# Performance work log

Hardware: AMD Instinct MI355X
Metric: run time of the kernel (lower is better)

The kernel has to match this reference:

```python
import jax, jax.numpy as jnp
import numpy as np

B, N, M, C = 32, 4096, 512, 256  # batch, grid points, retained modes, latent channels


def setup_inputs() -> dict:
    key = jax.random.key(0)
    k1, k2 = jax.random.split(key)
    v = jax.random.normal(k1, (B, N, C), dtype=jnp.float32)
    # glorot-style scale for a (C, C) per-mode transform: std = 1/sqrt(C)
    transform_R = jax.random.normal(k2, (M, C, C), dtype=jnp.float32) * np.float32(1.0 / np.sqrt(C))
    return {"v": v, "transform_R": transform_R}


def reference(v, transform_R):
    # v: (B, N, C) real; transform_R: (M, C, C) real, applied to complex modes
    n = v.shape[1]
    m = transform_R.shape[0]
    f = jnp.fft.rfft(v, axis=1)                     # (B, N//2+1, C) complex64
    fm = f[:, :m]                                   # keep low-frequency modes (B, M, C)
    # per-mode channel mixing: out[b,m,o] = sum_i R[m,i,o] * f[b,m,i]
    gm = jnp.einsum('mio,bmi->bmo', transform_R.astype(fm.dtype), fm)
    g = jnp.zeros_like(f).at[:, :m].set(gm)         # zero-pad high modes back
    return v + jnp.fft.irfft(g, n=n, axis=1)        # residual add, (B, N, C)
```

## Files before the change

### kernel.cpp

```cpp
#include <hip/hip_runtime.h>
#include <hip/hip_fp16.h>
#include <math.h>


constexpr int BB = 32;
constexpr int CC = 256;
constexpr int MM = 512;

constexpr float PI2_4096 = 1.5339807878856412e-3f;
constexpr float PI2_512  = 1.2271846303085130e-2f;
constexpr float PI2_64   = 9.8174770424681035e-2f;
constexpr float PI_4     = 0.78539816339744831f;

__device__ __forceinline__ float2 cadd(float2 a, float2 b){ return make_float2(a.x+b.x, a.y+b.y); }
__device__ __forceinline__ float2 csub(float2 a, float2 b){ return make_float2(a.x-b.x, a.y-b.y); }
__device__ __forceinline__ float2 cmulf(float2 a, float2 b){ return make_float2(a.x*b.x - a.y*b.y, a.x*b.y + a.y*b.x); }

template<int S>
__device__ __forceinline__ void dif8(float2 x[8]) {
    const float R = 0.70710678118654752f;
    const float Sf = (float)S;
    float2 a0=cadd(x[0],x[4]), a1=cadd(x[1],x[5]), a2=cadd(x[2],x[6]), a3=cadd(x[3],x[7]);
    float2 d0=csub(x[0],x[4]), d1=csub(x[1],x[5]), d2=csub(x[2],x[6]), d3=csub(x[3],x[7]);
    float2 t5 = cmulf(d1, make_float2(R, -R*Sf));
    float2 t6 = make_float2(Sf*d2.y, -Sf*d2.x);
    float2 t7 = cmulf(d3, make_float2(-R, -R*Sf));
    float2 b0=cadd(a0,a2), b1=cadd(a1,a3), b2=csub(a0,a2), e3=csub(a1,a3);
    float2 b3=make_float2(Sf*e3.y, -Sf*e3.x);
    float2 b4=cadd(d0,t6), b5=cadd(t5,t7), b6=csub(d0,t6), e7=csub(t5,t7);
    float2 b7=make_float2(Sf*e7.y, -Sf*e7.x);
    x[0]=cadd(b0,b1); x[4]=csub(b0,b1);
    x[2]=cadd(b2,b3); x[6]=csub(b2,b3);
    x[1]=cadd(b4,b5); x[5]=csub(b4,b5);
    x[3]=cadd(b6,b7); x[7]=csub(b6,b7);
}

__device__ __forceinline__ void twid7(float2 x[8], float ang) {
    float s, c;
    __sincosf(ang, &s, &c);
    float2 w = make_float2(c, s), cur = w;
    x[1] = cmulf(x[1], cur);
    #pragma unroll
    for (int k = 2; k < 8; ++k) { cur = cmulf(cur, w); x[k] = cmulf(x[k], cur); }
}

__global__ __launch_bounds__(256) void k1a_kernel(const float* __restrict__ v,
                                                  __half2* __restrict__ ybuf, int b0) {
    __shared__ float2 T[64 * 65];
    const int blk = blockIdx.x;
    const int ct = blk & 1;
    const int n2 = (blk >> 1) & 63;
    const int bl = blk >> 7;
    const int bat = b0 + bl;
    const int t = threadIdx.x;
    const int p = t & 63;
    const int g = t >> 6;

    const float* vb = v + ((size_t)bat << 20) + (size_t)n2 * CC + ct * 128 + 2 * p;
    float2 X[2][8];
    #pragma unroll
    for (int s = 0; s < 2; ++s) {
        const int bd = g + 4 * s;
        #pragma unroll
        for (int a = 0; a < 8; ++a)
            X[s][a] = *(const float2*)(vb + (size_t)(8 * a + bd) * 16384);
    }
    #pragma unroll
    for (int s = 0; s < 2; ++s) {
        const int bd = g + 4 * s;
        dif8<1>(X[s]);
        twid7(X[s], -PI2_64 * (float)bd);
        float2* row = T + p * 65;
        #pragma unroll
        for (int k0 = 0; k0 < 8; ++k0) row[bd + 8 * k0] = X[s][k0];
    }
    __syncthreads();

    __half2* yb = ybuf + (size_t)bl * (64 * 64 * 128) + ct * 64 + p;
    #pragma unroll
    for (int s = 0; s < 2; ++s) {
        const int k0 = g + 4 * s;
        float2 Y[8];
        const float2* row = T + p * 65 + 8 * k0;
        #pragma unroll
        for (int b = 0; b < 8; ++b) Y[b] = row[b];
        dif8<1>(Y);
        float bs, bc, ss, sc;
        __sincosf(-PI2_4096 * (float)(n2 * k0), &bs, &bc);
        __sincosf(-PI2_512 * (float)n2, &ss, &sc);
        float2 cur = make_float2(bc, bs), stp = make_float2(sc, ss);
        #pragma unroll
        for (int k1b = 0; k1b < 8; ++k1b) {
            float2 r = cmulf(Y[k1b], cur);
            yb[(size_t)((k0 + 8 * k1b) * 64 + n2) * 128] = __floats2half2_rn(r.x, r.y);
            cur = cmulf(cur, stp);
        }
    }
}

__global__ __launch_bounds__(256) void k1b_kernel(const __half2* __restrict__ ybuf,
                                                  __half2* __restrict__ zbuf, int b0) {
    __shared__ float2 T[64 * 65];
    const int blk = blockIdx.x;
    const int ct = blk & 1;
    const int k1 = (blk >> 1) & 63;
    const int bl = blk >> 7;
    const int bat = b0 + bl;
    const int t = threadIdx.x;
    const int p = t & 63;
    const int g = t >> 6;
    const float R = 0.70710678118654752f;

    const __half2* yb = ybuf + (size_t)bl * (64 * 64 * 128) + (size_t)k1 * (64 * 128) + ct * 64 + p;
    float2 X[2][8];
    #pragma unroll
    for (int s = 0; s < 2; ++s) {
        const int bd = g + 4 * s;
        #pragma unroll
        for (int a = 0; a < 8; ++a)
            X[s][a] = __half22float2(yb[(size_t)(8 * a + bd) * 128]);
    }
    #pragma unroll
    for (int s = 0; s < 2; ++s) {
        const int bd = g + 4 * s;
        dif8<1>(X[s]);
        twid7(X[s], -PI2_64 * (float)bd);
        float2* row = T + p * 65;
        #pragma unroll
        for (int k0 = 0; k0 < 8; ++k0) row[bd + 8 * k0] = X[s][k0];
    }
    __syncthreads();

    __half2* zb = zbuf + ((size_t)(bat * 64 + k1) * 16) * 128 + ct * 64 + p;
    #pragma unroll
    for (int s = 0; s < 2; ++s) {
        const int k20 = g + 4 * s;
        float2 r[8];
        const float2* row = T + p * 65 + 8 * k20;
        #pragma unroll
        for (int b = 0; b < 8; ++b) r[b] = row[b];
        float2 sum0 = make_float2(0.f, 0.f);
        #pragma unroll
        for (int b = 0; b < 8; ++b) sum0 = cadd(sum0, r[b]);
        float2 e0 = csub(r[0], r[4]);
        float2 e1 = csub(r[1], r[5]);
        float2 e2 = csub(r[2], r[6]);
        float2 e3 = csub(r[3], r[7]);
        float2 sum7 = cadd(cadd(e0, cmulf(e1, make_float2(R, R))),
                           cadd(make_float2(-e2.y, e2.x), cmulf(e3, make_float2(-R, R))));
        zb[(size_t)k20 * 128]       = __floats2half2_rn(sum0.x, sum0.y);
        zb[(size_t)(k20 + 8) * 128] = __floats2half2_rn(sum7.x, sum7.y);
    }
}

__global__ __launch_bounds__(256) void k2_kernel(const __half2* __restrict__ zbuf,
                                                 const float* __restrict__ R,
                                                 __half* __restrict__ gre,
                                                 __half* __restrict__ gim) {
    __shared__ __half XT[256 * 64];
    const int mh = blockIdx.x & 1;
    const int m  = blockIdx.x >> 1;
    const int t = threadIdx.x;
    const int k1 = m & 63, k2 = m >> 6;
    int k1p, jp;
    if (k1 == 0) { k1p = 0;       jp = (k2 == 0) ? 0 : (16 - k2); }
    else         { k1p = 64 - k1; jp = 15 - k2; }
    {
        const int b  = t & 31;
        const int pg = t >> 5;
        const __half2* zm = zbuf + ((size_t)(b * 64 + k1 ) * 16 + k2) * 128;
        const __half2* zp = zbuf + ((size_t)(b * 64 + k1p) * 16 + jp) * 128;
        #pragma unroll
        for (int q = 0; q < 16; ++q) {
            int pp = pg + 8 * q;
            float2 a = __half22float2(zm[pp]);
            float2 c = __half22float2(zp[pp]);
            XT[(2 * pp) * 64 + b]          = __float2half_rn(0.5f * (a.x + c.x));
            XT[(2 * pp) * 64 + 32 + b]     = __float2half_rn(0.5f * (a.y - c.y));
            XT[(2 * pp + 1) * 64 + b]      = __float2half_rn(0.5f * (a.y + c.y));
            XT[(2 * pp + 1) * 64 + 32 + b] = __float2half_rn(0.5f * (c.x - a.x));
        }
    }
    __syncthreads();

    const int rblk = t >> 4;
    const int ol   = t & 15;
    float4 acc[2][4];
    #pragma unroll
    for (int jj = 0; jj < 2; ++jj)
        #pragma unroll
        for (int rr = 0; rr < 4; ++rr) acc[jj][rr] = make_float4(0.f, 0.f, 0.f, 0.f);

    const float* Rb = R + (size_t)m * 65536 + mh * 128 + ol * 4;
    float4 c0 = *(const float4*)&Rb[0];
    float4 c1 = *(const float4*)&Rb[64];
    for (int i = 0; i < 256; ++i) {
        float4 n0 = c0, n1 = c1;
        if (i < 255) {
            n0 = *(const float4*)&Rb[(size_t)(i + 1) * 256];
            n1 = *(const float4*)&Rb[(size_t)(i + 1) * 256 + 64];
        }
        const __half2* xp = (const __half2*)&XT[i * 64 + rblk * 4];
        float2 x01 = __half22float2(xp[0]);
        float2 x23 = __half22float2(xp[1]);
        float xs[4] = {x01.x, x01.y, x23.x, x23.y};
        #pragma unroll
        for (int rr = 0; rr < 4; ++rr) {
            acc[0][rr].x += xs[rr] * c0.x; acc[0][rr].y += xs[rr] * c0.y;
            acc[0][rr].z += xs[rr] * c0.z; acc[0][rr].w += xs[rr] * c0.w;
            acc[1][rr].x += xs[rr] * c1.x; acc[1][rr].y += xs[rr] * c1.y;
            acc[1][rr].z += xs[rr] * c1.z; acc[1][rr].w += xs[rr] * c1.w;
        }
        c0 = n0; c1 = n1;
    }

    union U { __half2 h2[2]; float2 f2; };
    #pragma unroll
    for (int jj = 0; jj < 2; ++jj) {
        #pragma unroll
        for (int rr = 0; rr < 4; ++rr) {
            int r = rblk * 4 + rr;
            __half* plane = (r < 32) ? gre : gim;
            size_t off = ((size_t)m * BB + (r & 31)) * CC + mh * 128 + (ol + 16 * jj) * 4;
            U u;
            u.h2[0] = __floats2half2_rn(acc[jj][rr].x, acc[jj][rr].y);
            u.h2[1] = __floats2half2_rn(acc[jj][rr].z, acc[jj][rr].w);
            *(float2*)(plane + off) = u.f2;
        }
    }
}

__global__ __launch_bounds__(256) void k3a_kernel(const __half* __restrict__ gre,
                                                  const __half* __restrict__ gim,
                                                  __half2* __restrict__ tbuf, int b0) {
    const int blk = blockIdx.x;
    const int ct = blk & 1;
    const int k1 = (blk >> 1) & 63;
    const int bl = blk >> 7;
    const int bat = b0 + bl;
    const int t = threadIdx.x;
    const int p = t & 63;
    const int g = t >> 6;

    float2 Zd[8], Zc[8];
    #pragma unroll
    for (int k20 = 0; k20 < 8; ++k20) {
        int m = k1 + 64 * k20;
        size_t off = ((size_t)m * BB + bat) * CC + ct * 128 + 2 * p;
        float2 a = __half22float2(*(const __half2*)(gre + off));
        float2 c = __half22float2(*(const __half2*)(gim + off));
        Zd[k20] = make_float2(a.x - c.y, c.x + a.y);
        int mp = 512 - k1 - 64 * k20;
        if (mp != 512) {
            size_t offp = ((size_t)mp * BB + bat) * CC + ct * 128 + 2 * p;
            float2 ap = __half22float2(*(const __half2*)(gre + offp));
            float2 cp = __half22float2(*(const __half2*)(gim + offp));
            Zc[k20] = make_float2(ap.x + cp.y, ap.y - cp.x);
        } else {
            Zc[k20] = make_float2(0.f, 0.f);
        }
    }

    __half2* tb = tbuf + (size_t)bl * (64 * 64 * 128) + (size_t)k1 * 128 + ct * 64 + p;
    #pragma unroll
    for (int s = 0; s < 2; ++s) {
        const int bd = g + 4 * s;
        float w8s, w8c;
        __sincosf(-PI_4 * (float)bd, &w8s, &w8c);
        float2 u[8];
        #pragma unroll
        for (int k20 = 0; k20 < 8; ++k20)
            u[k20] = cadd(Zd[k20], cmulf(Zc[k20], make_float2(w8c, w8s)));
        twid7(u, PI2_64 * (float)bd);
        dif8<-1>(u);
        float bs, bc, ss, sc;
        __sincosf(PI2_4096 * (float)(bd * k1), &bs, &bc);
        __sincosf(PI2_512 * (float)k1, &ss, &sc);
        float2 cur = make_float2(bc, bs), stp = make_float2(sc, ss);
        #pragma unroll
        for (int a = 0; a < 8; ++a) {
            float2 r = cmulf(u[a], cur);
            tb[(size_t)(8 * a + bd) * (64 * 128)] = __floats2half2_rn(r.x, r.y);
            cur = cmulf(cur, stp);
        }
    }
}

__global__ __launch_bounds__(256) void k3b_kernel(const __half2* __restrict__ tbuf,
                                                  const float* __restrict__ v,
                                                  float* __restrict__ out, int b0) {
    __shared__ float2 T[64 * 65];
    const int blk = blockIdx.x;
    const int ct = blk & 1;
    const int n2 = (blk >> 1) & 63;
    const int bl = blk >> 7;
    const int bat = b0 + bl;
    const int t = threadIdx.x;
    const int p = t & 63;
    const int g = t >> 6;

    const __half2* tb = tbuf + (size_t)bl * (64 * 64 * 128) + (size_t)n2 * (64 * 128) + ct * 64 + p;
    float2 X[2][8];
    #pragma unroll
    for (int s = 0; s < 2; ++s) {
        const int be = g + 4 * s;
        #pragma unroll
        for (int a = 0; a < 8; ++a)
            X[s][a] = __half22float2(tb[(size_t)(8 * a + be) * 128]);
    }
    #pragma unroll
    for (int s = 0; s < 2; ++s) {
        const int be = g + 4 * s;
        dif8<-1>(X[s]);
        twid7(X[s], PI2_64 * (float)be);
        float2* row = T + p * 65;
        #pragma unroll
        for (int j0 = 0; j0 < 8; ++j0) row[be + 8 * j0] = X[s][j0];
    }
    __syncthreads();

    const float sc = 1.0f / 4096.0f;
    const float* vb = v   + ((size_t)bat << 20) + (size_t)n2 * CC + ct * 128 + 2 * p;
    float*       ob = out + ((size_t)bat << 20) + (size_t)n2 * CC + ct * 128 + 2 * p;
    #pragma unroll
    for (int s = 0; s < 2; ++s) {
        const int j0 = g + 4 * s;
        float2 r[8];
        const float2* row = T + p * 65 + 8 * j0;
        #pragma unroll
        for (int b = 0; b < 8; ++b) r[b] = row[b];
        dif8<-1>(r);
        #pragma unroll
        for (int j1 = 0; j1 < 8; ++j1) {
            int n1 = j0 + 8 * j1;
            size_t off = (size_t)n1 * 16384;
            float2 vz = *(const float2*)(vb + off);
            float2 o = make_float2(vz.x + r[j1].x * sc, vz.y + r[j1].y * sc);
            *(float2*)(ob + off) = o;
        }
    }
}

extern "C" void kernel_launch(void* const* d_in, const int* in_sizes, int n_in,
                              void* d_out, int out_size, void* d_ws, size_t ws_size,
                              hipStream_t stream) {
    const float* v = (const float*)d_in[0];
    const float* R = (const float*)d_in[1];
    float* out = (float*)d_out;

    __half2* ybuf = (__half2*)d_ws;
    __half2* zbuf = ybuf + (size_t)16 * 64 * 64 * 128;
    __half*  gre  = (__half*)(zbuf + (size_t)32 * 64 * 16 * 128);
    __half*  gim  = gre + (size_t)MM * BB * CC;

    for (int h = 0; h < 2; ++h) {
        k1a_kernel<<<2048, 256, 0, stream>>>(v, ybuf, h * 16);
        k1b_kernel<<<2048, 256, 0, stream>>>(ybuf, zbuf, h * 16);
    }
    k2_kernel<<<1024, 256, 0, stream>>>(zbuf, R, gre, gim);
    for (int h = 0; h < 2; ++h) {
        k3a_kernel<<<2048, 256, 0, stream>>>(gre, gim, ybuf, h * 16);
        k3b_kernel<<<2048, 256, 0, stream>>>(ybuf, v, out, h * 16);
    }
}
```

Before: 485.7 us.

## Use fp16 MFMA with split hi/lo weights for per-mode channel mixing

Replaces the scalar FMA loop in the per-mode channel-mixing kernel with MFMA 16x16x32 fp16 instructions. The activation tile is stored transposed in shared memory with an XOR swizzle to avoid bank conflicts. The fp32 weights are split into high and low fp16 parts so two MFMAs keep roughly fp32 accuracy. The aim is to move the matmul onto the matrix cores instead of the vector ALUs. In exchange it adds strided, uncoalesced weight loads and scalar half stores on output.

```diff
diff --git a/kernel.cpp b/kernel.cpp
--- a/kernel.cpp
+++ b/kernel.cpp
@@ -11,6 +11,9 @@
 constexpr float PI2_512  = 1.2271846303085130e-2f;
 constexpr float PI2_64   = 9.8174770424681035e-2f;
 constexpr float PI_4     = 0.78539816339744831f;
+
+typedef _Float16 f16x8 __attribute__((ext_vector_type(8)));
+typedef float f32x4 __attribute__((ext_vector_type(4)));
 
 __device__ __forceinline__ float2 cadd(float2 a, float2 b){ return make_float2(a.x+b.x, a.y+b.y); }
 __device__ __forceinline__ float2 csub(float2 a, float2 b){ return make_float2(a.x-b.x, a.y-b.y); }
@@ -153,11 +156,15 @@
     }
 }
 
+__device__ __forceinline__ int swzh(int r, int col) {
+    return r * 256 + (col ^ ((r & 7) << 3));
+}
+
 __global__ __launch_bounds__(256) void k2_kernel(const __half2* __restrict__ zbuf,
                                                  const float* __restrict__ R,
                                                  __half* __restrict__ gre,
                                                  __half* __restrict__ gim) {
-    __shared__ __half XT[256 * 64];
+    __shared__ __align__(16) __half XT[64 * 256];
     const int mh = blockIdx.x & 1;
     const int m  = blockIdx.x >> 1;
     const int t = threadIdx.x;
@@ -175,57 +182,64 @@
             int pp = pg + 8 * q;
             float2 a = __half22float2(zm[pp]);
             float2 c = __half22float2(zp[pp]);
-            XT[(2 * pp) * 64 + b]          = __float2half_rn(0.5f * (a.x + c.x));
-            XT[(2 * pp) * 64 + 32 + b]     = __float2half_rn(0.5f * (a.y - c.y));
-            XT[(2 * pp + 1) * 64 + b]      = __float2half_rn(0.5f * (a.y + c.y));
-            XT[(2 * pp + 1) * 64 + 32 + b] = __float2half_rn(0.5f * (c.x - a.x));
+            *(__half2*)&XT[swzh(b,      2 * pp)] = __floats2half2_rn(0.5f * (a.x + c.x), 0.5f * (a.y + c.y));
+            *(__half2*)&XT[swzh(b + 32, 2 * pp)] = __floats2half2_rn(0.5f * (a.y - c.y), 0.5f * (c.x - a.x));
         }
     }
     __syncthreads();
 
-    const int rblk = t >> 4;
-    const int ol   = t & 15;
-    float4 acc[2][4];
-    #pragma unroll
-    for (int jj = 0; jj < 2; ++jj)
-        #pragma unroll
-        for (int rr = 0; rr < 4; ++rr) acc[jj][rr] = make_float4(0.f, 0.f, 0.f, 0.f);
-
-    const float* Rb = R + (size_t)m * 65536 + mh * 128 + ol * 4;
-    float4 c0 = *(const float4*)&Rb[0];
-    float4 c1 = *(const float4*)&Rb[64];
-    for (int i = 0; i < 256; ++i) {
-        float4 n0 = c0, n1 = c1;
-        if (i < 255) {
-            n0 = *(const float4*)&Rb[(size_t)(i + 1) * 256];
-            n1 = *(const float4*)&Rb[(size_t)(i + 1) * 256 + 64];
-        }
-        const __half2* xp = (const __half2*)&XT[i * 64 + rblk * 4];
-        float2 x01 = __half22float2(xp[0]);
-        float2 x23 = __half22float2(xp[1]);
-        float xs[4] = {x01.x, x01.y, x23.x, x23.y};
-        #pragma unroll
-        for (int rr = 0; rr < 4; ++rr) {
-            acc[0][rr].x += xs[rr] * c0.x; acc[0][rr].y += xs[rr] * c0.y;
-            acc[0][rr].z += xs[rr] * c0.z; acc[0][rr].w += xs[rr] * c0.w;
-            acc[1][rr].x += xs[rr] * c1.x; acc[1][rr].y += xs[rr] * c1.y;
-            acc[1][rr].z += xs[rr] * c1.z; acc[1][rr].w += xs[rr] * c1.w;
-        }
-        c0 = n0; c1 = n1;
-    }
-
-    union U { __half2 h2[2]; float2 f2; };
-    #pragma unroll
-    for (int jj = 0; jj < 2; ++jj) {
-        #pragma unroll
-        for (int rr = 0; rr < 4; ++rr) {
-            int r = rblk * 4 + rr;
-            __half* plane = (r < 32) ? gre : gim;
-            size_t off = ((size_t)m * BB + (r & 31)) * CC + mh * 128 + (ol + 16 * jj) * 4;
-            U u;
-            u.h2[0] = __floats2half2_rn(acc[jj][rr].x, acc[jj][rr].y);
-            u.h2[1] = __floats2half2_rn(acc[jj][rr].z, acc[jj][rr].w);
-            *(float2*)(plane + off) = u.f2;
+    const int w  = t >> 6;
+    const int l  = t & 63;
+    const int lr = l & 15;
+    const int kg = l >> 4;
+    const int colbase = mh * 128 + w * 32;
+
+    f32x4 acc[4][2];
+    #pragma unroll
+    for (int mt = 0; mt < 4; ++mt)
+        #pragma unroll
+        for (int nt = 0; nt < 2; ++nt)
+            acc[mt][nt] = (f32x4){0.f, 0.f, 0.f, 0.f};
+
+    const float* Rb = R + (size_t)m * 65536 + colbase + lr;
+
+    for (int kt = 0; kt < 8; ++kt) {
+        f16x8 afrag[4];
+        #pragma unroll
+        for (int mt = 0; mt < 4; ++mt)
+            afrag[mt] = *(const f16x8*)&XT[swzh(mt * 16 + lr, kt * 32 + kg * 8)];
+        #pragma unroll
+        for (int nt = 0; nt < 2; ++nt) {
+            const float* rp = Rb + (size_t)(kt * 32 + kg * 8) * 256 + nt * 16;
+            float rv[8];
+            #pragma unroll
+            for (int j = 0; j < 8; ++j) rv[j] = rp[(size_t)j * 256];
+            f16x8 bhi, blo;
+            #pragma unroll
+            for (int j = 0; j < 8; ++j) {
+                _Float16 h = (_Float16)rv[j];
+                bhi[j] = h;
+                blo[j] = (_Float16)(rv[j] - (float)h);
+            }
+            #pragma unroll
+            for (int mt = 0; mt < 4; ++mt) {
+                acc[mt][nt] = __builtin_amdgcn_mfma_f32_16x16x32_f16(afrag[mt], bhi, acc[mt][nt], 0, 0, 0);
+                acc[mt][nt] = __builtin_amdgcn_mfma_f32_16x16x32_f16(afrag[mt], blo, acc[mt][nt], 0, 0, 0);
+            }
+        }
+    }
+
+    #pragma unroll
+    for (int mt = 0; mt < 4; ++mt) {
+        __half* plane = (mt < 2) ? gre : gim;
+        const int bb = (mt & 1) * 16 + kg * 4;
+        #pragma unroll
+        for (int nt = 0; nt < 2; ++nt) {
+            const int n = colbase + nt * 16 + lr;
+            #pragma unroll
+            for (int j = 0; j < 4; ++j) {
+                plane[((size_t)m * BB + (bb + j)) * CC + n] = __float2half_rn(acc[mt][nt][j]);
+            }
         }
     }
 }
```

Result: faster. 427.7 us (-11.9%).
